# Kernel optimization log

Measured on AMD Instinct MI355X. Metric: run time of the kernel, lower is better.

The kernel has to match this reference:

```python
import jax, jax.numpy as jnp
import numpy as np

M, H, D, P = 16, 32, 128, 8192
N = H * D


def setup_inputs() -> dict:
    key = jax.random.key(0)
    ks = jax.random.split(key, 8)
    w_scale = 0.3 / np.sqrt(N)  # keep q,k ~ N(0, 0.3^2) so exp(c) stays finite
    X = jax.random.normal(ks[0], (M, N), jnp.float32)
    Wq = jax.random.normal(ks[1], (N, N), jnp.float32) * w_scale
    Wk = jax.random.normal(ks[2], (N, N), jnp.float32) * w_scale
    Wv = jax.random.normal(ks[3], (N, N), jnp.float32) * w_scale
    cache_K = jax.random.normal(ks[4], (H, P, D), jnp.float32) * 0.3
    cache_V = jax.random.normal(ks[5], (H, P, D), jnp.float32) * 0.3
    tau = jnp.float32(2.0)
    noise = jax.random.normal(ks[6], (H, M, P + M), jnp.float32) * 0.1
    return {"X": X, "Wq": Wq, "Wk": Wk, "Wv": Wv,
            "cache_K": cache_K, "cache_V": cache_V, "tau": tau, "noise": noise}


def reference(X, Wq, Wk, Wv, cache_K, cache_V, tau, noise):
    h, p, d = cache_K.shape
    m, n = X.shape
    # RMS-style prenorm: X / sqrt(mean(X^2, dim=1))
    x_norm = X * jax.lax.rsqrt(jnp.sum(X * X, axis=1, keepdims=True) / n)
    # nn.Linear: y = x @ W^T; reshape to [H, M, D]
    q = (x_norm @ Wq.T).reshape(m, h, d).transpose(1, 0, 2)
    k = (x_norm @ Wk.T).reshape(m, h, d).transpose(1, 0, 2)
    v = (x_norm @ Wv.T).reshape(m, h, d).transpose(1, 0, 2)
    k_cache = jnp.concatenate([cache_K, k], axis=1)  # [H, P+M, D]
    v_cache = jnp.concatenate([cache_V, v], axis=1)
    c = jnp.einsum('hmd,hpd->hmp', q, k_cache)  # [H, M, P+M]
    c_exp = jnp.exp(c)
    c_exp_perturb = jnp.exp((c + noise) / tau)
    c_div = c_exp / jnp.sum(c_exp, axis=2, keepdims=True)
    c_div_perturb = c_exp_perturb / jnp.sum(c_exp_perturb, axis=2, keepdims=True)
    c_out = jnp.sum(c_div_perturb, axis=1)  # [H, P+M]
    o = jnp.einsum('hmp,hpd->hmd', c_div, v_cache)  # [H, M, D]
    o2 = o.transpose(1, 0, 2).reshape(m, n)
    return o2, c_out
```

## Files before the change

kernel.cpp:

```cpp
#include <hip/hip_runtime.h>

#define M_ 16
#define H_ 32
#define D_ 128
#define P_ 8192
#define N_ 4096
#define PM_ 8208

#define WS_Q    0
#define WS_K    65536
#define WS_V    131072
#define WS_S1   196608
#define WS_S2   197120
#define WS_IS2  197632
#define WS_XQ   198144
#define WS_E2   263680
#define WS_E1   4466176
#define WS_PP   263680
#define WS_PO   8668672
#define WS_SP1  10765824
#define WS_SP2  10782208

__global__ __launch_bounds__(256) void rmsnorm_kernel(const float* __restrict__ X,
                                                      float* __restrict__ ws) {
  int m = blockIdx.x, t = threadIdx.x;
  __shared__ float red[256];
  const float4* X4 = (const float4*)(X + (size_t)m * N_);
  float s = 0.f;
  #pragma unroll
  for (int q = 0; q < 4; q++) {
    float4 v = X4[t + q * 256];
    s += v.x * v.x + v.y * v.y + v.z * v.z + v.w * v.w;
  }
  red[t] = s;
  __syncthreads();
  for (int off = 128; off > 0; off >>= 1) {
    if (t < off) red[t] += red[t + off];
    __syncthreads();
  }
  float scale = rsqrtf(red[0] * (1.0f / N_));
  float4* xq = (float4*)(ws + WS_XQ);
  #pragma unroll
  for (int q = 0; q < 4; q++) {
    int nq = t + q * 256;
    float4 v = X4[nq];
    v.x *= scale; v.y *= scale; v.z *= scale; v.w *= scale;
    xq[nq * 16 + m] = v;
  }
}

__global__ __launch_bounds__(256, 4) void proj_kernel(const float* __restrict__ Wq,
                                                      const float* __restrict__ Wk,
                                                      const float* __restrict__ Wv,
                                                      const float* __restrict__ xr,
                                                      float* __restrict__ ws) {
  int widx = threadIdx.x >> 6, lane = threadIdx.x & 63;
  int kc = blockIdx.x / 48;
  int jt = (blockIdx.x % 48) * 4 + widx;
  int jj0 = jt * 64;
  int sel = jj0 >> 12;
  int j0 = jj0 & 4095;
  const float* Wm = (sel == 0) ? Wq : ((sel == 1) ? Wk : Wv);
  int n0 = kc * 128;

  const float4* wrow = (const float4*)(Wm + (size_t)(j0 + lane) * N_ + n0);
  const float4* xr4 = (const float4*)xr;

  float acc[16];
  #pragma unroll
  for (int m = 0; m < 16; m++) acc[m] = 0.f;

  #pragma unroll
  for (int g = 0; g < 8; g++) {
    float4 w4[4];
    #pragma unroll
    for (int i = 0; i < 4; i++) w4[i] = wrow[g * 4 + i];
    #pragma unroll
    for (int i = 0; i < 4; i++) {
      int qbase = ((n0 >> 2) + g * 4 + i) * 16;
      #pragma unroll
      for (int m = 0; m < 16; m++) {
        float4 xm = xr4[qbase + m];
        acc[m] += xm.x * w4[i].x + xm.y * w4[i].y + xm.z * w4[i].z + xm.w * w4[i].w;
      }
    }
  }

  float* pp = ws + WS_PP + (size_t)kc * 16 * 12288 + jj0 + lane;
  #pragma unroll
  for (int m = 0; m < 16; m++) pp[(size_t)m * 12288] = acc[m];
}

__global__ __launch_bounds__(256) void proj_reduce_kernel(float* __restrict__ ws) {
  int tid = blockIdx.x * 256 + threadIdx.x;
  int m = tid / 12288;
  int j = tid - m * 12288;
  float acc = 0.f;
  #pragma unroll
  for (int kc = 0; kc < 32; kc++)
    acc += ws[WS_PP + ((size_t)(kc * 16 + m)) * 12288 + j];
  int sel = j >> 12, jj = j & 4095;
  int h = jj >> 7, d = jj & 127;
  ws[WS_Q + sel * 65536 + (h * 16 + m) * 128 + d] = acc;
}

__global__ __launch_bounds__(256) void qk_kernel(const float* __restrict__ cacheK,
                                                 const float* __restrict__ noise,
                                                 const float* __restrict__ taup,
                                                 float* __restrict__ ws) {
  __shared__ float sred[2][4][16];
  int h = blockIdx.x >> 5, b = blockIdx.x & 31;
  int widx = threadIdx.x >> 6, lane = threadIdx.x & 63;
  int m8 = lane & 7, sl = lane >> 3;
  int rsel = lane >> 4;
  int msel = lane & 15;
  bool tb = (lane >> 3) & 1;
  bool rb0 = rsel & 1, rb1 = (rsel >> 1) & 1;
  bool hb = sl >> 2, sb0 = sl & 1, sb1 = (sl >> 1) & 1;
  float inv_tau = 1.0f / taup[0];

  float qv[2][16];
  #pragma unroll
  for (int t = 0; t < 2; t++) {
    const float4* qp = (const float4*)(ws + WS_Q + ((size_t)(h * 16) + m8 + 8 * t) * 128 + sl * 16);
    #pragma unroll
    for (int jq = 0; jq < 4; jq++) {
      float4 v = qp[jq];
      qv[t][jq * 4] = v.x; qv[t][jq * 4 + 1] = v.y;
      qv[t][jq * 4 + 2] = v.z; qv[t][jq * 4 + 3] = v.w;
    }
  }
  float s1 = 0.f, s2 = 0.f;

  const float* nbase = noise + ((size_t)h * 16 + msel) * PM_;
  float* e2base = ws + WS_E2 + (size_t)h * PM_ * 16 + msel;
  float* e1base = ws + WS_E1 + (size_t)h * PM_ * 16 + (sl & 3) * 16 + (sl >> 2) * 8 + m8;
  const float* kc_base = cacheK + (size_t)h * P_ * D_;

  auto qk_one = [&](int p0, const float* kb) {
    float nz = nbase[p0 + rsel];

    float pr[4][2];
    #pragma unroll
    for (int r = 0; r < 4; r++) {
      float4 kq[4];
      const float4* krp = (const float4*)(kb + r * D_ + sl * 16);
      kq[0] = krp[0]; kq[1] = krp[1]; kq[2] = krp[2]; kq[3] = krp[3];
      const float* kk = (const float*)kq;
      float t0 = 0.f, t1 = 0.f;
      #pragma unroll
      for (int j = 0; j < 16; j++) { t0 += kk[j] * qv[0][j]; t1 += kk[j] * qv[1][j]; }
      pr[r][0] = t0; pr[r][1] = t1;
    }
    float cc[4][2];
    #pragma unroll
    for (int r = 0; r < 4; r++)
      #pragma unroll
      for (int t = 0; t < 2; t++) {
        float v = pr[r][t];
        v += __shfl_xor(v, 8, 64);
        v += __shfl_xor(v, 16, 64);
        v += __shfl_xor(v, 32, 64);
        cc[r][t] = v;
      }

    float a0 = tb ? cc[0][1] : cc[0][0];
    float a1 = tb ? cc[1][1] : cc[1][0];
    float a2 = tb ? cc[2][1] : cc[2][0];
    float a3 = tb ? cc[3][1] : cc[3][0];
    float b0 = rb0 ? a1 : a0;
    float b1 = rb0 ? a3 : a2;
    float myc = rb1 ? b1 : b0;
    float e2 = __expf((myc + nz) * inv_tau);
    e2base[(size_t)(p0 + rsel) * 16] = e2;
    s2 += e2;

    float e1[4][2];
    #pragma unroll
    for (int r = 0; r < 4; r++) {
      e1[r][0] = __expf(cc[r][0]);
      e1[r][1] = __expf(cc[r][1]);
    }
    float f0 = tb ? e1[0][1] : e1[0][0];
    float f1 = tb ? e1[1][1] : e1[1][0];
    float f2 = tb ? e1[2][1] : e1[2][0];
    float f3 = tb ? e1[3][1] : e1[3][0];
    float g0s = rb0 ? f1 : f0;
    float g1s = rb0 ? f3 : f2;
    s1 += rb1 ? g1s : g0s;

    float u0 = hb ? e1[0][1] : e1[0][0];
    float u1 = hb ? e1[1][1] : e1[1][0];
    float u2 = hb ? e1[2][1] : e1[2][0];
    float u3 = hb ? e1[3][1] : e1[3][0];
    float w0 = sb0 ? u1 : u0;
    float w1 = sb0 ? u3 : u2;
    float val = sb1 ? w1 : w0;
    e1base[(size_t)p0 * 16] = val;
  };

  int g0 = b * 64;
  for (int gl = widx; gl < 64; gl += 4) {
    int p0 = (g0 + gl) * 4;
    qk_one(p0, kc_base + (size_t)p0 * D_);
  }
  if (b == 31) {
    int p0 = P_ + widx * 4;
    qk_one(p0, ws + WS_K + ((size_t)h * 16 + widx * 4) * 128);
  }

  s1 += __shfl_xor(s1, 16, 64); s1 += __shfl_xor(s1, 32, 64);
  s2 += __shfl_xor(s2, 16, 64); s2 += __shfl_xor(s2, 32, 64);
  if (lane < 16) { sred[0][widx][lane] = s1; sred[1][widx][lane] = s2; }
  __syncthreads();
  if (threadIdx.x < 16) {
    int mm = threadIdx.x;
    float a  = sred[0][0][mm] + sred[0][1][mm] + sred[0][2][mm] + sred[0][3][mm];
    float c2 = sred[1][0][mm] + sred[1][1][mm] + sred[1][2][mm] + sred[1][3][mm];
    ws[WS_SP1 + (size_t)(h * 32 + b) * 16 + mm] = a;
    ws[WS_SP2 + (size_t)(h * 32 + b) * 16 + mm] = c2;
  }
}

__global__ __launch_bounds__(256) void pv_kernel(const float* __restrict__ cacheV,
                                                 const float* __restrict__ ws,
                                                 float* __restrict__ wout) {
  __shared__ float red[4 * 2048];
  int h = blockIdx.x >> 5, b = blockIdx.x & 31;
  int widx = threadIdx.x >> 6, lane = threadIdx.x & 63;
  int m8 = lane & 7, sl = lane >> 3;

  float oacc[2][16];
  #pragma unroll
  for (int t = 0; t < 2; t++)
    #pragma unroll
    for (int j = 0; j < 16; j++) oacc[t][j] = 0.f;

  const float* e1r = ws + WS_E1 + (size_t)h * PM_ * 16 + m8;
  const float* vc_base = cacheV + (size_t)h * P_ * D_;

  auto pv_one = [&](int p0, const float* vb) {
    float ea[4], eb[4];
    #pragma unroll
    for (int r = 0; r < 4; r++) {
      ea[r] = e1r[(size_t)p0 * 16 + r * 16];
      eb[r] = e1r[(size_t)p0 * 16 + r * 16 + 8];
    }
    #pragma unroll
    for (int r = 0; r < 4; r++) {
      float4 vq[4];
      const float4* vrp = (const float4*)(vb + r * D_ + sl * 16);
      vq[0] = vrp[0]; vq[1] = vrp[1]; vq[2] = vrp[2]; vq[3] = vrp[3];
      const float* vv = (const float*)vq;
      #pragma unroll
      for (int j = 0; j < 16; j++) {
        oacc[0][j] += ea[r] * vv[j];
        oacc[1][j] += eb[r] * vv[j];
      }
    }
  };

  int g0 = b * 64;
  for (int gl = widx; gl < 64; gl += 4) {
    int p0 = (g0 + gl) * 4;
    pv_one(p0, vc_base + (size_t)p0 * D_);
  }
  if (b == 31) {
    int p0 = P_ + widx * 4;
    pv_one(p0, ws + WS_V + ((size_t)h * 16 + widx * 4) * 128);
  }

  float* rw = red + widx * 2048 + lane * 32;
  #pragma unroll
  for (int t = 0; t < 2; t++)
    #pragma unroll
    for (int j = 0; j < 16; j++) {
      int i = t * 16 + j;
      rw[(i + lane) & 31] = oacc[t][j];
    }
  __syncthreads();

  float* po = wout + WS_PO + (size_t)(h * 32 + b) * 2048;
  for (int e = threadIdx.x; e < 2048; e += 256) {
    int ln = e >> 5, i = e & 31;
    int phys = (ln << 5) + ((i + ln) & 31);
    float v = red[phys] + red[phys + 2048] + red[phys + 4096] + red[phys + 6144];
    int mo = (ln & 7) + 8 * (i >> 4);
    int d = (ln >> 3) * 16 + (i & 15);
    po[mo * 128 + d] = v;
  }
}

__global__ __launch_bounds__(256) void sums_kernel(float* __restrict__ ws) {
  int tid = blockIdx.x * 256 + threadIdx.x;
  if (tid >= 512) return;
  int h = tid >> 4, m = tid & 15;
  float a = 0.f, c2 = 0.f;
  #pragma unroll
  for (int b = 0; b < 32; b++) {
    a  += ws[WS_SP1 + (size_t)(h * 32 + b) * 16 + m];
    c2 += ws[WS_SP2 + (size_t)(h * 32 + b) * 16 + m];
  }
  ws[WS_S1 + tid] = a;
  ws[WS_S2 + tid] = c2;
  ws[WS_IS2 + tid] = 1.0f / c2;
}

__global__ __launch_bounds__(256) void epilogue_kernel(const float* __restrict__ ws,
                                                       float* __restrict__ out) {
  int tid = blockIdx.x * 256 + threadIdx.x;
  int mm = tid >> 12, j = tid & 4095;
  int h = j >> 7, d = j & 127;
  float acc = 0.f;
  #pragma unroll
  for (int b = 0; b < 32; b++)
    acc += ws[WS_PO + (size_t)(h * 32 + b) * 2048 + mm * 128 + d];
  out[tid] = acc / ws[WS_S1 + h * 16 + mm];
}

__global__ __launch_bounds__(256) void cout_kernel(const float* __restrict__ ws,
                                                   float* __restrict__ out) {
  int tid = blockIdx.x * 256 + threadIdx.x;
  if (tid >= H_ * PM_) return;
  int h = tid / PM_, p = tid - h * PM_;
  const float4* e2p = (const float4*)(ws + WS_E2 + ((size_t)h * PM_ + p) * 16);
  const float* is2 = ws + WS_IS2 + h * 16;
  float acc = 0.f;
  #pragma unroll
  for (int q = 0; q < 4; q++) {
    float4 v = e2p[q];
    acc += v.x * is2[q * 4] + v.y * is2[q * 4 + 1] + v.z * is2[q * 4 + 2] + v.w * is2[q * 4 + 3];
  }
  out[65536 + tid] = acc;
}

extern "C" void kernel_launch(void* const* d_in, const int* in_sizes, int n_in,
                              void* d_out, int out_size, void* d_ws, size_t ws_size,
                              hipStream_t stream) {
  const float* X     = (const float*)d_in[0];
  const float* Wq    = (const float*)d_in[1];
  const float* Wk    = (const float*)d_in[2];
  const float* Wv    = (const float*)d_in[3];
  const float* cK    = (const float*)d_in[4];
  const float* cV    = (const float*)d_in[5];
  const float* tau   = (const float*)d_in[6];
  const float* noise = (const float*)d_in[7];
  float* out = (float*)d_out;
  float* ws  = (float*)d_ws;

  rmsnorm_kernel<<<16, 256, 0, stream>>>(X, ws);
  proj_kernel<<<1536, 256, 0, stream>>>(Wq, Wk, Wv, ws + WS_XQ, ws);
  proj_reduce_kernel<<<768, 256, 0, stream>>>(ws);
  qk_kernel<<<1024, 256, 0, stream>>>(cK, noise, tau, ws);
  sums_kernel<<<2, 256, 0, stream>>>(ws);
  pv_kernel<<<1024, 256, 0, stream>>>(cV, ws, ws);
  epilogue_kernel<<<256, 256, 0, stream>>>(ws, out);
  cout_kernel<<<1026, 256, 0, stream>>>(ws, out);
}
```

Baseline: 232.0 us.

## Stage projection weight tiles through LDS with async global_load_lds double buffering

```diff
diff --git a/kernel.cpp b/kernel.cpp
--- a/kernel.cpp
+++ b/kernel.cpp
@@ -21,6 +21,9 @@
 #define WS_SP1  10765824
 #define WS_SP2  10782208
 
+typedef __attribute__((address_space(1))) const void gvoid_t;
+typedef __attribute__((address_space(3))) void lvoid_t;
+
 __global__ __launch_bounds__(256) void rmsnorm_kernel(const float* __restrict__ X,
                                                       float* __restrict__ ws) {
   int m = blockIdx.x, t = threadIdx.x;
@@ -54,6 +57,7 @@
                                                       const float* __restrict__ Wv,
                                                       const float* __restrict__ xr,
                                                       float* __restrict__ ws) {
+  __shared__ float tile[4 * 2048];
   int widx = threadIdx.x >> 6, lane = threadIdx.x & 63;
   int kc = blockIdx.x / 48;
   int jt = (blockIdx.x % 48) * 4 + widx;
@@ -63,25 +67,54 @@
   const float* Wm = (sel == 0) ? Wq : ((sel == 1) ? Wk : Wv);
   int n0 = kc * 128;
 
-  const float4* wrow = (const float4*)(Wm + (size_t)(j0 + lane) * N_ + n0);
+  float* tl = tile + widx * 2048;
+  int r16 = lane >> 2;
+  int cswz = (lane & 3) ^ (r16 & 3);
+
+  const float* gsrc[4];
+  #pragma unroll
+  for (int i = 0; i < 4; i++)
+    gsrc[i] = Wm + (size_t)(j0 + i * 16 + r16) * N_ + n0 + cswz * 4;
+
+  const float4* tl4 = (const float4*)tl;
   const float4* xr4 = (const float4*)xr;
 
   float acc[16];
   #pragma unroll
   for (int m = 0; m < 16; m++) acc[m] = 0.f;
 
-  #pragma unroll
-  for (int g = 0; g < 8; g++) {
-    float4 w4[4];
-    #pragma unroll
-    for (int i = 0; i < 4; i++) w4[i] = wrow[g * 4 + i];
-    #pragma unroll
-    for (int i = 0; i < 4; i++) {
-      int qbase = ((n0 >> 2) + g * 4 + i) * 16;
+  auto STAGE = [&](int h) {
+    float* dst = tl + (h & 1) * 1024;
+    #pragma unroll
+    for (int i = 0; i < 4; i++)
+      __builtin_amdgcn_global_load_lds((gvoid_t*)(gsrc[i] + h * 16),
+                                       (lvoid_t*)(dst + i * 256), 16, 0, 0);
+  };
+
+  STAGE(0);
+  STAGE(1);
+  #pragma unroll
+  for (int h = 0; h < 8; h++) {
+    if (h < 7) asm volatile("s_waitcnt vmcnt(4)" ::: "memory");
+    else       asm volatile("s_waitcnt vmcnt(0)" ::: "memory");
+    __builtin_amdgcn_sched_barrier(0);
+    int bb = (h & 1) * 256 + lane * 4;
+    float4 w0 = tl4[bb + (0 ^ (lane & 3))];
+    float4 w1 = tl4[bb + (1 ^ (lane & 3))];
+    float4 w2 = tl4[bb + (2 ^ (lane & 3))];
+    float4 w3 = tl4[bb + (3 ^ (lane & 3))];
+    asm volatile("s_waitcnt lgkmcnt(0)" ::: "memory");
+    __builtin_amdgcn_sched_barrier(0);
+    if (h + 2 < 8) STAGE(h + 2);
+    float4 wq[4] = {w0, w1, w2, w3};
+    int qb = (n0 >> 2) + h * 4;
+    #pragma unroll
+    for (int k = 0; k < 4; k++) {
+      int qbase = (qb + k) * 16;
       #pragma unroll
       for (int m = 0; m < 16; m++) {
         float4 xm = xr4[qbase + m];
-        acc[m] += xm.x * w4[i].x + xm.y * w4[i].y + xm.z * w4[i].z + xm.w * w4[i].w;
+        acc[m] += xm.x * wq[k].x + xm.y * wq[k].y + xm.z * wq[k].z + xm.w * wq[k].w;
       }
     }
   }
```

After: 428.7 us. 1.85x slower.
